# Kernel optimization log

Hardware: AMD Instinct MI355X
Metric: run time of the kernel (lower is better)

## Reference

```python
import jax, jax.numpy as jnp
import numpy as np

N, E, H, K = 50000, 300000, 128, 50
PI = float(np.pi)
EPS = 1e-5


def gaussian_expand(ea, k):
    # RBF expansion of each edge feature into k gaussians on [0, 1]
    centers = jnp.linspace(0.0, 1.0, k)            # (k,)
    width = 1.0 / k
    g = jnp.exp(-((ea[..., None] - centers) ** 2) / (2.0 * width * width))  # (E, 4, k)
    return g.reshape(ea.shape[0], -1)              # (E, 4k)


def bn_train(z, g, b):
    # BatchNorm1d in training mode: biased batch stats
    m = jnp.mean(z, axis=0)
    v = jnp.mean(z * z, axis=0) - m * m
    return (z - m) * jax.lax.rsqrt(v + EPS) * g + b


def lrelu(z):
    return jnp.where(z >= 0, z, 0.01 * z)


def setup_inputs() -> dict:
    key = jax.random.key(0)
    ks = jax.random.split(key, 16)
    s = 0.02
    d = {
        "x": jax.random.normal(ks[0], (N, H), jnp.float32),
        "edge_attr": jax.random.uniform(ks[1], (E, 4), jnp.float32),
        "edge_index": jax.random.randint(ks[2], (2, E), 0, N, jnp.int32),
        # f_b: Linear(4K -> H)
        "Wb": jax.random.normal(ks[3], (4 * K, H), jnp.float32) * s,
        "bb": jnp.zeros((H,), jnp.float32),
        # f_e: Linear(3H->H) + LReLU + BN + Linear(H->H) + LReLU + BN + Linear(H->H)
        "We1": jax.random.normal(ks[4], (3 * H, H), jnp.float32) * s,
        "be1": jnp.zeros((H,), jnp.float32),
        "ge1": jnp.ones((H,), jnp.float32),
        "bte1": jnp.zeros((H,), jnp.float32),
        "We2": jax.random.normal(ks[5], (H, H), jnp.float32) * s,
        "be2": jnp.zeros((H,), jnp.float32),
        "ge2": jnp.ones((H,), jnp.float32),
        "bte2": jnp.zeros((H,), jnp.float32),
        "We3": jax.random.normal(ks[6], (H, H), jnp.float32) * s,
        "be3": jnp.zeros((H,), jnp.float32),
        # f_d: Linear(H->H)
        "Wd": jax.random.normal(ks[7], (H, H), jnp.float32) * s,
        "bd": jnp.zeros((H,), jnp.float32),
        # v parameter (1, H)
        "v": jnp.ones((1, H), jnp.float32),
        # f_n: Linear(H->H) + LReLU + BN + Linear(H->H)
        "Wn1": jax.random.normal(ks[8], (H, H), jnp.float32) * s,
        "bn1": jnp.zeros((H,), jnp.float32),
        "gn": jnp.ones((H,), jnp.float32),
        "btn": jnp.zeros((H,), jnp.float32),
        "Wn2": jax.random.normal(ks[9], (H, H), jnp.float32) * s,
        "bn2": jnp.zeros((H,), jnp.float32),
    }
    return d


def reference(x, edge_attr, edge_index, Wb, bb, We1, be1, ge1, bte1, We2, be2,
              ge2, bte2, We3, be3, Wd, bd, v, Wn1, bn1, gn, btn, Wn2, bn2):
    src, dst = edge_index[0], edge_index[1]
    gt = gaussian_expand(edge_attr, K) @ Wb + bb            # (E, H)
    coeff = jnp.cos(PI / 2 * edge_attr[:, 3])[:, None]      # (E, 1)
    h = jnp.concatenate([x[src], gt, x[dst]], axis=1)       # (E, 3H)
    h = bn_train(lrelu(h @ We1 + be1), ge1, bte1)
    h = bn_train(lrelu(h @ We2 + be2), ge2, bte2)
    cond_filter = coeff * (h @ We3 + be3)                   # (E, H)
    m_st = cond_filter * (x[src] @ Wd + bd)                 # (E, H)
    m_t = v * (x @ Wd + bd)                                 # (N, H)
    incoming = jax.ops.segment_sum(m_st, dst, num_segments=N)  # scatter_add + zero pad
    z = m_t + incoming
    out = bn_train(lrelu(z @ Wn1 + bn1), gn, btn) @ Wn2 + bn2 + x
    return out
```

## Files before the change

kernel.cpp:

```cpp
#include <hip/hip_runtime.h>

typedef __attribute__((ext_vector_type(8))) short bf16x8;
typedef __attribute__((ext_vector_type(4))) float f32x4;

#define DEVFN __device__ __forceinline__

DEVFN short f2bf(float f) {
    union { float f; unsigned u; } v; v.f = f;
    unsigned r = (v.u + 0x7FFFu + ((v.u >> 16) & 1u)) >> 16;
    return (short)(unsigned short)r;
}
DEVFN float bf2f(short h) {
    union { unsigned u; float f; } v; v.u = ((unsigned)(unsigned short)h) << 16;
    return v.f;
}
DEVFN unsigned packbf(float a, float b) {
    return (unsigned)(unsigned short)f2bf(a) | ((unsigned)(unsigned short)f2bf(b) << 16);
}

#define GLD_LDS16(gp, lp)                                                     \
    __builtin_amdgcn_global_load_lds(                                         \
        (const __attribute__((address_space(1))) unsigned*)(gp),              \
        (__attribute__((address_space(3))) unsigned*)(lp), 16, 0, 0)



__global__ __launch_bounds__(128) void build_w1p_k(
    const float* __restrict__ Wb, const float* __restrict__ We1,
    const float* __restrict__ bb, const float* __restrict__ be1,
    float* __restrict__ W1p, float* __restrict__ b1p)
{
    int j = threadIdx.x;
    const float* B = We1 + 128 * 128;
    int i = blockIdx.x;
    if (i < 200) {
        float a = 0.f;
        for (int m = 0; m < 128; m++) a += Wb[i * 128 + m] * B[m * 128 + j];
        W1p[i * 128 + j] = a;
    } else {
        float a = be1[j];
        for (int m = 0; m < 128; m++) a += bb[m] * B[m * 128 + j];
        b1p[j] = a;
    }
}

__global__ __launch_bounds__(128) void build_tab_k(
    const float* __restrict__ W1p, const float* __restrict__ b1p,
    short* __restrict__ tab)
{
    int i = blockIdx.x;
    int c = blockIdx.y;
    int j = threadIdx.x;
    float t = (float)i * (1.0f / 1024.0f);
    float acc = (c == 0) ? b1p[j] : 0.f;
    int kc = (int)(t * 49.f + 0.5f);
    for (int dk = -6; dk <= 6; dk++) {
        int k = kc + dk;
        if (k >= 0 && k < 50) {
            float d = t - (float)k * (1.f / 49.f);
            float g = expf(-1250.f * d * d);
            acc += g * W1p[(c * 50 + k) * 128 + j];
        }
    }
    tab[((size_t)(c * 1025 + i)) * 128 + j] = f2bf(acc);
}

__global__ __launch_bounds__(256) void fold_plain_k(
    const float* __restrict__ W0, const float* __restrict__ W1,
    const float* __restrict__ W2, const float* __restrict__ W3,
    short* __restrict__ O0, short* __restrict__ O1,
    short* __restrict__ O2, short* __restrict__ O3)
{
    const float* W = (blockIdx.y == 0) ? W0 : (blockIdx.y == 1) ? W1 : (blockIdx.y == 2) ? W2 : W3;
    short* O = (blockIdx.y == 0) ? O0 : (blockIdx.y == 1) ? O1 : (blockIdx.y == 2) ? O2 : O3;
    int idx = blockIdx.x * 256 + threadIdx.x;
    int n = idx >> 8, ks = (idx >> 6) & 3, lane = idx & 63;
    int k8 = ks * 32 + (lane >> 4) * 8;
    int pcol = (lane & 15) * 8 + n;
    bf16x8 fv;
    #pragma unroll
    for (int i2 = 0; i2 < 8; i2++) fv[i2] = f2bf(W[(k8 + i2) * 128 + pcol]);
    *(bf16x8*)(O + (size_t)idx * 8) = fv;
}

__global__ __launch_bounds__(256) void fold_k(
    const float* __restrict__ W, const float* __restrict__ bias,
    const float* __restrict__ statsG, const float* __restrict__ gamma,
    const float* __restrict__ beta, float invNs,
    short* __restrict__ Bp, float* __restrict__ biasOut)
{
    __shared__ float sS[128], sT[128];
    int tid = threadIdx.x;
    if (tid < 128) {
        float sum = 0.f, sq = 0.f;
        for (int r = 0; r < 16; r++) {
            sum += statsG[r * 256 + tid];
            sq  += statsG[r * 256 + 128 + tid];
        }
        float m = sum * invNs;
        float var = sq * invNs - m * m;
        float rs = rsqrtf(var + 1e-5f);
        float s = rs * gamma[tid];
        float t = beta[tid] - m * s;
        sS[tid] = s; sT[tid] = t;
    }
    __syncthreads();
    if (blockIdx.x == 0 && tid < 128) {
        float b = bias[tid];
        for (int k = 0; k < 128; k++) b += sT[k] * W[k * 128 + tid];
        biasOut[tid] = b;
    }
    int idx = blockIdx.x * 256 + tid;
    int n = idx >> 8, ks = (idx >> 6) & 3, lane = idx & 63;
    int k8 = ks * 32 + (lane >> 4) * 8;
    int pcol = (lane & 15) * 8 + n;
    bf16x8 fv;
    #pragma unroll
    for (int i2 = 0; i2 < 8; i2++)
        fv[i2] = f2bf(sS[k8 + i2] * W[(k8 + i2) * 128 + pcol]);
    *(bf16x8*)(Bp + (size_t)idx * 8) = fv;
}


__global__ __launch_bounds__(256) void hist_k(
    const int* __restrict__ dstI, int* __restrict__ cnt, int E)
{
    int e = blockIdx.x * 256 + threadIdx.x;
    if (e < E) atomicAdd(&cnt[dstI[e]], 1);
}

__global__ __launch_bounds__(256) void scan1_k(
    const int* __restrict__ cnt, int Nn, int* __restrict__ posE, int* __restrict__ bsum)
{
    __shared__ int s[256];
    int t = threadIdx.x, g = blockIdx.x * 256 + t;
    int v = (g < Nn) ? cnt[g] : 0;
    s[t] = v;
    __syncthreads();
    for (int off = 1; off < 256; off <<= 1) {
        int u = (t >= off) ? s[t - off] : 0;
        __syncthreads();
        s[t] += u;
        __syncthreads();
    }
    if (g < Nn) posE[g] = s[t] - v;
    if (t == 255) bsum[blockIdx.x] = s[255];
}

__global__ __launch_bounds__(256) void scan2_k(int* __restrict__ bsum, int nb)
{
    __shared__ int s[256];
    int t = threadIdx.x;
    int v = (t < nb) ? bsum[t] : 0;
    s[t] = v;
    __syncthreads();
    for (int off = 1; off < 256; off <<= 1) {
        int u = (t >= off) ? s[t - off] : 0;
        __syncthreads();
        s[t] += u;
        __syncthreads();
    }
    if (t < nb) bsum[t] = s[t] - v;
}

__global__ __launch_bounds__(256) void fix_k(
    const int* __restrict__ posE, const int* __restrict__ bsum,
    int* __restrict__ pos2, int Nn)
{
    int id = blockIdx.x * 256 + threadIdx.x;
    if (id < Nn) pos2[id] = posE[id] + bsum[id >> 8];
}

__global__ __launch_bounds__(256) void scat_k(
    const int* __restrict__ srcI, const int* __restrict__ dstI,
    const float4* __restrict__ ea4, int* __restrict__ pos2,
    int* __restrict__ sSrc, int* __restrict__ sDst,
    float* __restrict__ scf, float4* __restrict__ sEa, int E)
{
    int e = blockIdx.x * 256 + threadIdx.x;
    if (e >= E) return;
    int d = dstI[e];
    int p = atomicAdd(&pos2[d], 1);
    sSrc[p] = srcI[e];
    sDst[p] = d;
    float4 ev = ea4[e];
    sEa[p] = ev;
    scf[p] = cosf(1.57079632679f * ev.w);
}

__global__ __launch_bounds__(256, 4) void node_all_k(
    const float* __restrict__ x, int M,
    const short* __restrict__ bp3,
    const float* __restrict__ bd, const float* __restrict__ vv,
    short* __restrict__ xd, short* __restrict__ zaccb,
    short* __restrict__ xs1b, short* __restrict__ xt1b)
{
    int tid = threadIdx.x;
    int wave = tid >> 6, lane = tid & 63;
    int kgrp = lane >> 4, colbase = lane & 15;
    int chunk = blockIdx.x;
    int rowA = chunk * 64 + wave * 16 + colbase;
    bool rv = rowA < M;

    bf16x8 af[4];
    #pragma unroll
    for (int ks = 0; ks < 4; ks++) {
        bf16x8 v = (bf16x8){0,0,0,0,0,0,0,0};
        if (rv) {
            const float* ap = x + (size_t)rowA * 128 + ks * 32 + kgrp * 8;
            float4 f0 = ((const float4*)ap)[0];
            float4 f1 = ((const float4*)ap)[1];
            v[0] = f2bf(f0.x); v[1] = f2bf(f0.y); v[2] = f2bf(f0.z); v[3] = f2bf(f0.w);
            v[4] = f2bf(f1.x); v[5] = f2bf(f1.y); v[6] = f2bf(f1.z); v[7] = f2bf(f1.w);
        }
        af[ks] = v;
    }

    float bcol[8], vcol[8];
    *(float4*)&bcol[0] = *(const float4*)(bd + colbase * 8);
    *(float4*)&bcol[4] = *(const float4*)(bd + colbase * 8 + 4);
    *(float4*)&vcol[0] = *(const float4*)(vv + colbase * 8);
    *(float4*)&vcol[4] = *(const float4*)(vv + colbase * 8 + 4);

    int rbase = chunk * 64 + wave * 16 + kgrp * 4;

    for (int b = 0; b < 3; b++) {
        const short* Bb = bp3 + (size_t)b * 16384;
        f32x4 acc[8];
        #pragma unroll
        for (int n = 0; n < 8; n++) acc[n] = (f32x4){0.f, 0.f, 0.f, 0.f};
        #pragma unroll
        for (int ks = 0; ks < 4; ks++) {
            #pragma unroll
            for (int n = 0; n < 8; n++) {
                bf16x8 bf = *(const bf16x8*)(Bb + ((size_t)((n * 4 + ks) * 64 + lane)) * 8);
                acc[n] = __builtin_amdgcn_mfma_f32_16x16x32_bf16(af[ks], bf, acc[n], 0, 0, 0);
            }
        }
        if (b == 0) {
            #pragma unroll
            for (int r = 0; r < 4; r++) {
                int row = rbase + r;
                if (row < M) {
                    bf16x8 xo, zo;
                    #pragma unroll
                    for (int n = 0; n < 8; n++) {
                        float val = acc[n][r] + bcol[n];
                        xo[n] = f2bf(val);
                        zo[n] = f2bf(vcol[n] * val);
                    }
                    *(bf16x8*)(xd    + (size_t)row * 128 + colbase * 8) = xo;
                    *(bf16x8*)(zaccb + (size_t)row * 128 + colbase * 8) = zo;
                }
            }
        } else {
            short* outp = (b == 1) ? xs1b : xt1b;
            #pragma unroll
            for (int r = 0; r < 4; r++) {
                int row = rbase + r;
                if (row < M) {
                    bf16x8 o;
                    #pragma unroll
                    for (int n = 0; n < 8; n++) o[n] = f2bf(acc[n][r]);
                    *(bf16x8*)(outp + (size_t)row * 128 + colbase * 8) = o;
                }
            }
        }
    }
}

__global__ __launch_bounds__(256) void edge_z1_k(
    const short* __restrict__ xs1b, const short* __restrict__ xt1b,
    const short* __restrict__ tab,
    const int* __restrict__ sSrc, const int* __restrict__ sDst,
    const float4* __restrict__ sEa,
    short* __restrict__ z1, float* __restrict__ stats, int Etot)
{
    int tid = threadIdx.x, wave = tid >> 6, lane = tid & 63;
    int colg = lane & 15, esub = lane >> 4;
    int e0 = blockIdx.x * 256 + wave * 64;

    int eL = e0 + lane;
    int myS = 0, myD = 0;
    float4 myE = {0.f, 0.f, 0.f, 0.f};
    if (eL < Etot) { myS = sSrc[eL]; myD = sDst[eL]; myE = sEa[eL]; }

    float sacc[8], qacc[8];
    #pragma unroll
    for (int j = 0; j < 8; j++) { sacc[j] = 0.f; qacc[j] = 0.f; }

    int ni = Etot - e0; if (ni > 64) ni = 64;
    int nsteps = (ni + 3) >> 2;

    for (int st = 0; st < nsteps; st++) {
        int i = st * 4 + esub;
        bool valid = i < ni;
        int s = __shfl(myS, i);
        int d = __shfl(myD, i);
        float tv[4];
        tv[0] = __shfl(myE.x, i); tv[1] = __shfl(myE.y, i);
        tv[2] = __shfl(myE.z, i); tv[3] = __shfl(myE.w, i);

        bf16x8 xs8 = *(const bf16x8*)(xs1b + (size_t)s * 128 + colg * 8);
        bf16x8 xt8 = *(const bf16x8*)(xt1b + (size_t)d * 128 + colg * 8);

        float p[8];
        #pragma unroll
        for (int j = 0; j < 8; j++) p[j] = bf2f(xs8[j]) + bf2f(xt8[j]);

        #pragma unroll
        for (int c = 0; c < 4; c++) {
            float u = tv[c] * 1024.f;
            int i0 = (int)u;
            if (i0 > 1023) i0 = 1023;
            if (i0 < 0) i0 = 0;
            float f = u - (float)i0;
            const short* tb = tab + ((size_t)(c * 1025 + i0)) * 128 + colg * 8;
            bf16x8 t0 = *(const bf16x8*)tb;
            bf16x8 t1 = *(const bf16x8*)(tb + 128);
            #pragma unroll
            for (int j = 0; j < 8; j++) {
                float v0 = bf2f(t0[j]);
                p[j] += v0 + f * (bf2f(t1[j]) - v0);
            }
        }

        bf16x8 o;
        #pragma unroll
        for (int j = 0; j < 8; j++) {
            float z = p[j] >= 0.f ? p[j] : 0.01f * p[j];
            o[j] = f2bf(z);
            if (valid) { sacc[j] += z; qacc[j] += z * z; }
        }
        if (valid)
            *(bf16x8*)(z1 + (size_t)(e0 + i) * 128 + colg * 8) = o;
    }

    __shared__ float lS[128], lQ[128];
    if (tid < 128) { lS[tid] = 0.f; lQ[tid] = 0.f; }
    __syncthreads();
    #pragma unroll
    for (int j = 0; j < 8; j++) {
        atomicAdd(&lS[colg * 8 + j], sacc[j]);
        atomicAdd(&lQ[colg * 8 + j], qacc[j]);
    }
    __syncthreads();
    if (tid < 128) {
        int rep = blockIdx.x & 15;
        atomicAdd(&stats[rep * 256 + tid], lS[tid]);
        atomicAdd(&stats[rep * 256 + 128 + tid], lQ[tid]);
    }
}

__global__ __launch_bounds__(256) void segred_k(
    const short* __restrict__ cond, const short* __restrict__ xd,
    const int* __restrict__ sSrc, const int* __restrict__ endPos,
    short* __restrict__ zaccb, int Nn)
{
    int tid = threadIdx.x, wave = tid >> 6, lane = tid & 63;
    int colg = lane & 7;
    int esub = lane >> 3;
    int d0 = blockIdx.x * 64 + wave * 16;

    for (int i = 0; i < 16; i++) {
        int d = d0 + i;
        if (d >= Nn) break;
        int s0 = (d == 0) ? 0 : endPos[d - 1];
        int s1 = endPos[d];
        if (s1 <= s0) continue;

        float acc[16];
        #pragma unroll
        for (int j = 0; j < 16; j++) acc[j] = 0.f;

        for (int t = s0 + esub; t < s1; t += 8) {
            const short* cp = cond + (size_t)t * 128 + colg * 16;
            bf16x8 c0 = *(const bf16x8*)cp;
            bf16x8 c1 = *(const bf16x8*)(cp + 8);
            int s = sSrc[t];
            const short* xp = xd + (size_t)s * 128 + colg * 16;
            bf16x8 x0 = *(const bf16x8*)xp;
            bf16x8 x1 = *(const bf16x8*)(xp + 8);
            #pragma unroll
            for (int j = 0; j < 8; j++) {
                acc[j]     += bf2f(c0[j]) * bf2f(x0[j]);
                acc[8 + j] += bf2f(c1[j]) * bf2f(x1[j]);
            }
        }

        #pragma unroll
        for (int j = 0; j < 16; j++) {
            acc[j] += __shfl_xor(acc[j], 8);
            acc[j] += __shfl_xor(acc[j], 16);
            acc[j] += __shfl_xor(acc[j], 32);
        }

        if (esub == 0) {
            short* zp = zaccb + (size_t)d * 128 + colg * 16;
            bf16x8 z0 = *(const bf16x8*)zp;
            bf16x8 z1 = *(const bf16x8*)(zp + 8);
            bf16x8 o0, o1;
            #pragma unroll
            for (int j = 0; j < 8; j++) {
                o0[j] = f2bf(bf2f(z0[j]) + acc[j]);
                o1[j] = f2bf(bf2f(z1[j]) + acc[8 + j]);
            }
            *(bf16x8*)zp = o0;
            *(bf16x8*)(zp + 8) = o1;
        }
    }
}

template<int EPI>
__global__ __launch_bounds__(256, 2) void pgemm_k(
    const short* __restrict__ A, int M,
    const short* __restrict__ Bp, const float* __restrict__ bias,
    void* __restrict__ out, float* __restrict__ stats,
    const short* __restrict__ xd, short* __restrict__ zaccb,
    const float* __restrict__ scf, const int* __restrict__ sSrc,
    const int* __restrict__ sDst, const float* __restrict__ xres)
{
    __shared__ __align__(16) short ldsB[16384];
    __shared__ float lS[128], lQ[128];
    int tid = threadIdx.x;
    int wave = tid >> 6, lane = tid & 63;
    int kgrp = lane >> 4, colbase = lane & 15;

    #pragma unroll
    for (int i = 0; i < 8; i++) {
        int off = (i * 256 + wave * 64 + lane) * 8;
        GLD_LDS16(Bp + off, ldsB + off);
    }

    int nch = (M + 63) >> 6;
    int c = blockIdx.x;

    bf16x8 afc[4];
    {
        int rowA = c * 64 + wave * 16 + colbase;
        bool rv = (c < nch) && (rowA < M);
        #pragma unroll
        for (int ks = 0; ks < 4; ks++)
            afc[ks] = rv ? *(const bf16x8*)(A + (size_t)rowA * 128 + ks * 32 + kgrp * 8)
                         : (bf16x8){0,0,0,0,0,0,0,0};
    }

    float bcol[8];
    *(float4*)&bcol[0] = *(const float4*)(bias + colbase * 8);
    *(float4*)&bcol[4] = *(const float4*)(bias + colbase * 8 + 4);

    float sreg[8], qreg[8];
    if (EPI == 2) {
        #pragma unroll
        for (int n = 0; n < 8; n++) { sreg[n] = 0.f; qreg[n] = 0.f; }
        if (tid < 128) { lS[tid] = 0.f; lQ[tid] = 0.f; }
    }

    __syncthreads();

    for (; c < nch; c += gridDim.x) {
        int cn = c + gridDim.x;
        bf16x8 afn[4];
        {
            int rowA = cn * 64 + wave * 16 + colbase;
            bool rv = (cn < nch) && (rowA < M);
            #pragma unroll
            for (int ks = 0; ks < 4; ks++)
                afn[ks] = rv ? *(const bf16x8*)(A + (size_t)rowA * 128 + ks * 32 + kgrp * 8)
                             : (bf16x8){0,0,0,0,0,0,0,0};
        }

        int rbase = c * 64 + wave * 16 + kgrp * 4;

        float mcf[4];
        if (EPI == 3) {
            #pragma unroll
            for (int r = 0; r < 4; r++) {
                int row = rbase + r;
                mcf[r] = (row < M) ? scf[row] : 0.f;
            }
        }

        f32x4 acc[8];
        #pragma unroll
        for (int n = 0; n < 8; n++) acc[n] = (f32x4){0.f, 0.f, 0.f, 0.f};
        #pragma unroll
        for (int ks = 0; ks < 4; ks++) {
            #pragma unroll
            for (int n = 0; n < 8; n++) {
                bf16x8 bf = *(const bf16x8*)(ldsB + ((size_t)((n * 4 + ks) * 64 + lane)) * 8);
                acc[n] = __builtin_amdgcn_mfma_f32_16x16x32_bf16(afc[ks], bf, acc[n], 0, 0, 0);
            }
        }

        if (EPI == 2) {
            short* outh = (short*)out;
            #pragma unroll
            for (int r = 0; r < 4; r++) {
                int row = rbase + r;
                bf16x8 o;
                #pragma unroll
                for (int n = 0; n < 8; n++) {
                    float z = acc[n][r] + bcol[n];
                    z = z >= 0.f ? z : 0.01f * z;
                    if (row >= M) z = 0.f;
                    sreg[n] += z; qreg[n] += z * z;
                    o[n] = f2bf(z);
                }
                if (row < M)
                    *(bf16x8*)(outh + (size_t)row * 128 + colbase * 8) = o;
            }
        } else if (EPI == 3) {
            short* outh = (short*)out;
            #pragma unroll
            for (int r = 0; r < 4; r++) {
                int row = rbase + r;
                if (row < M) {
                    bf16x8 o;
                    #pragma unroll
                    for (int n = 0; n < 8; n++)
                        o[n] = f2bf(mcf[r] * (acc[n][r] + bcol[n]));
                    *(bf16x8*)(outh + (size_t)row * 128 + colbase * 8) = o;
                }
            }
        } else if (EPI == 4) {
            float* outf = (float*)out;
            #pragma unroll
            for (int r = 0; r < 4; r++) {
                int row = rbase + r;
                if (row < M) {
                    const float4* xr = (const float4*)(xres + (size_t)row * 128 + colbase * 8);
                    float4 x0 = xr[0], x1 = xr[1];
                    float4 o0, o1;
                    o0.x = acc[0][r] + bcol[0] + x0.x;
                    o0.y = acc[1][r] + bcol[1] + x0.y;
                    o0.z = acc[2][r] + bcol[2] + x0.z;
                    o0.w = acc[3][r] + bcol[3] + x0.w;
                    o1.x = acc[4][r] + bcol[4] + x1.x;
                    o1.y = acc[5][r] + bcol[5] + x1.y;
                    o1.z = acc[6][r] + bcol[6] + x1.z;
                    o1.w = acc[7][r] + bcol[7] + x1.w;
                    float4* op = (float4*)(outf + (size_t)row * 128 + colbase * 8);
                    op[0] = o0; op[1] = o1;
                }
            }
        }

        #pragma unroll
        for (int ks = 0; ks < 4; ks++) afc[ks] = afn[ks];
    }

    if (EPI == 2) {
        __syncthreads();
        #pragma unroll
        for (int n = 0; n < 8; n++) {
            atomicAdd(&lS[colbase * 8 + n], sreg[n]);
            atomicAdd(&lQ[colbase * 8 + n], qreg[n]);
        }
        __syncthreads();
        if (tid < 128) {
            int rep = blockIdx.x & 15;
            atomicAdd(&stats[rep * 256 + tid], lS[tid]);
            atomicAdd(&stats[rep * 256 + 128 + tid], lQ[tid]);
        }
    }
}

extern "C" void kernel_launch(void* const* d_in, const int* in_sizes, int n_in,
                              void* d_out, int out_size, void* d_ws, size_t ws_size,
                              hipStream_t stream)
{
    const float* x    = (const float*)d_in[0];
    const float* ea   = (const float*)d_in[1];
    const int*   eidx = (const int*)d_in[2];
    const float* Wb   = (const float*)d_in[3];
    const float* bb   = (const float*)d_in[4];
    const float* We1  = (const float*)d_in[5];
    const float* be1  = (const float*)d_in[6];
    const float* ge1  = (const float*)d_in[7];
    const float* bte1 = (const float*)d_in[8];
    const float* We2  = (const float*)d_in[9];
    const float* be2  = (const float*)d_in[10];
    const float* ge2  = (const float*)d_in[11];
    const float* bte2 = (const float*)d_in[12];
    const float* We3  = (const float*)d_in[13];
    const float* be3  = (const float*)d_in[14];
    const float* Wd   = (const float*)d_in[15];
    const float* bd   = (const float*)d_in[16];
    const float* vv   = (const float*)d_in[17];
    const float* Wn1  = (const float*)d_in[18];
    const float* bn1  = (const float*)d_in[19];
    const float* gn   = (const float*)d_in[20];
    const float* btn  = (const float*)d_in[21];
    const float* Wn2  = (const float*)d_in[22];
    const float* bn2  = (const float*)d_in[23];

    const int NN = in_sizes[0] / 128;
    const int EE = in_sizes[1] / 4;

    char* ws = (char*)d_ws;
    size_t oEZ   = 0;
    size_t oXD   = oEZ   + (size_t)EE * 256;
    size_t oXS   = oXD   + (size_t)NN * 256;
    size_t oXT   = oXS   + (size_t)NN * 256;
    size_t oZACC = oXT   + (size_t)NN * 256;
    size_t oZN   = oZACC + (size_t)NN * 256;
    size_t oTAB  = oZN   + (size_t)NN * 256;
    size_t oW1P  = oTAB  + (size_t)4 * 1025 * 256;
    size_t oB1P  = oW1P  + (size_t)200 * 512;
    size_t oBP   = oB1P  + 512;
    size_t oBIAS = oBP   + (size_t)7 * 32768;
    size_t oST   = oBIAS + (size_t)7 * 512;
    size_t oCNT  = oST   + 49152;
    size_t oPOS  = oCNT  + 201728;
    size_t oBSUM = oPOS  + 201728;
    size_t oPOS2 = oBSUM + 1024;
    size_t oSSRC = oPOS2 + 201728;
    size_t oSDST = oSSRC + (size_t)EE * 4;
    size_t oSCF  = oSDST + (size_t)EE * 4;
    size_t oSEA  = (oSCF + (size_t)EE * 4 + 15) & ~(size_t)15;

    short* eZ    = (short*)(ws + oEZ);
    short* xd    = (short*)(ws + oXD);
    short* xs1b  = (short*)(ws + oXS);
    short* xt1b  = (short*)(ws + oXT);
    short* zaccb = (short*)(ws + oZACC);
    short* zn    = (short*)(ws + oZN);
    short* tab   = (short*)(ws + oTAB);
    float* W1p   = (float*)(ws + oW1P);
    float* b1p   = (float*)(ws + oB1P);
    short* bp    = (short*)(ws + oBP);
    short* BpW2  = bp + 3 * 16384;
    short* BpW3  = bp + 4 * 16384;
    short* BpN1  = bp + 5 * 16384;
    short* BpN2  = bp + 6 * 16384;
    float* bo    = (float*)(ws + oBIAS);
    float* b2p   = bo + 0 * 128;
    float* b3p   = bo + 1 * 128;
    float* b2np  = bo + 2 * 128;
    float* st1   = (float*)(ws + oST);
    float* st2   = st1 + 4096;
    float* stN   = st1 + 8192;
    int*   cnt   = (int*)(ws + oCNT);
    int*   posE  = (int*)(ws + oPOS);
    int*   bsum  = (int*)(ws + oBSUM);
    int*   pos2  = (int*)(ws + oPOS2);
    int*   sSrc  = (int*)(ws + oSSRC);
    int*   sDst  = (int*)(ws + oSDST);
    float* scf   = (float*)(ws + oSCF);
    float4* sEa  = (float4*)(ws + oSEA);

    hipMemsetAsync(ws + oST, 0, 49152 + 201728, stream);

    build_w1p_k<<<201, 128, 0, stream>>>(Wb, We1, bb, be1, W1p, b1p);
    build_tab_k<<<dim3(1025, 4), 128, 0, stream>>>(W1p, b1p, tab);
    fold_plain_k<<<dim3(8, 4), 256, 0, stream>>>(
        Wd, We1, We1 + 256 * 128, Wn1, bp, bp + 16384, bp + 2 * 16384, BpN1);

    int nchN = (NN + 63) / 64;
    int nchE = (EE + 63) / 64;
    int nbN = (NN + 255) / 256;
    int nbE = (EE + 255) / 256;
    int nbSeg = (NN + 63) / 64;

    int gridE = nchE < 1024 ? nchE : 1024;
    int gridN = nchN < 512 ? nchN : 512;

    node_all_k<<<nchN, 256, 0, stream>>>(x, NN, bp, bd, vv, xd, zaccb, xs1b, xt1b);

    hist_k<<<nbE, 256, 0, stream>>>(eidx + EE, cnt, EE);
    scan1_k<<<nbN, 256, 0, stream>>>(cnt, NN, posE, bsum);
    scan2_k<<<1, 256, 0, stream>>>(bsum, nbN);
    fix_k<<<nbN, 256, 0, stream>>>(posE, bsum, pos2, NN);
    scat_k<<<nbE, 256, 0, stream>>>(eidx, eidx + EE, (const float4*)ea, pos2,
                                    sSrc, sDst, scf, sEa, EE);

    edge_z1_k<<<nbE, 256, 0, stream>>>(xs1b, xt1b, tab, sSrc, sDst, sEa, eZ, st1, EE);

    fold_k<<<8, 256, 0, stream>>>(We2, be2, st1, ge1, bte1, 1.f / (float)EE, BpW2, b2p);
    pgemm_k<2><<<gridE, 256, 0, stream>>>(eZ, EE, BpW2, b2p, eZ, st2,
        nullptr, nullptr, nullptr, nullptr, nullptr, nullptr);

    fold_k<<<8, 256, 0, stream>>>(We3, be3, st2, ge2, bte2, 1.f / (float)EE, BpW3, b3p);
    pgemm_k<3><<<gridE, 256, 0, stream>>>(eZ, EE, BpW3, b3p, eZ, nullptr,
        nullptr, nullptr, scf, nullptr, nullptr, nullptr);

    segred_k<<<nbSeg, 256, 0, stream>>>(eZ, xd, sSrc, pos2, zaccb, NN);

    pgemm_k<2><<<gridN, 256, 0, stream>>>(zaccb, NN, BpN1, bn1, zn, stN,
        nullptr, nullptr, nullptr, nullptr, nullptr, nullptr);

    fold_k<<<8, 256, 0, stream>>>(Wn2, bn2, stN, gn, btn, 1.f / (float)NN, BpN2, b2np);
    pgemm_k<4><<<gridN, 256, 0, stream>>>(zn, NN, BpN2, b2np, d_out, nullptr,
        nullptr, nullptr, nullptr, nullptr, nullptr, x);
}
```

Measured before the change: 437.3 us.

## Pack interpolation table as value+delta, software-pipeline edge loads, use packed bf16 convert

The Gaussian lookup table now stores each entry as a bf16 value paired with a bf16 delta to the next entry. Each interpolation therefore needs one contiguous 32-bit fetch per column instead of two separate row reads, and the lerp becomes a single fma. The edge_z1 kernel double-buffers its gathers, issuing loads for the next edge step before consuming the current one to hide gather latency. It also reads indices directly instead of through shuffles. Output packing in this kernel and the GEMM epilogues switches to the hardware v_cvt_pk_bf16_f32 instruction, at the cost of more registers and slightly different rounding of the delta.

```diff
diff --git a/kernel.cpp b/kernel.cpp
--- a/kernel.cpp
+++ b/kernel.cpp
@@ -2,6 +2,7 @@
 
 typedef __attribute__((ext_vector_type(8))) short bf16x8;
 typedef __attribute__((ext_vector_type(4))) float f32x4;
+typedef __attribute__((ext_vector_type(4))) unsigned uint32x4;
 
 #define DEVFN __device__ __forceinline__
 
@@ -14,8 +15,10 @@
     union { unsigned u; float f; } v; v.u = ((unsigned)(unsigned short)h) << 16;
     return v.f;
 }
-DEVFN unsigned packbf(float a, float b) {
-    return (unsigned)(unsigned short)f2bf(a) | ((unsigned)(unsigned short)f2bf(b) << 16);
+DEVFN unsigned pkbf(float a, float b) {
+    unsigned r;
+    asm("v_cvt_pk_bf16_f32 %0, %1, %2" : "=v"(r) : "v"(a), "v"(b));
+    return r;
 }
 
 #define GLD_LDS16(gp, lp)                                                     \
@@ -46,23 +49,31 @@
 
 __global__ __launch_bounds__(128) void build_tab_k(
     const float* __restrict__ W1p, const float* __restrict__ b1p,
-    short* __restrict__ tab)
+    unsigned* __restrict__ tabP)
 {
     int i = blockIdx.x;
     int c = blockIdx.y;
     int j = threadIdx.x;
-    float t = (float)i * (1.0f / 1024.0f);
-    float acc = (c == 0) ? b1p[j] : 0.f;
-    int kc = (int)(t * 49.f + 0.5f);
-    for (int dk = -6; dk <= 6; dk++) {
+    float t0 = (float)i * (1.0f / 1024.0f);
+    float t1 = (float)(i + 1) * (1.0f / 1024.0f);
+    float base = (c == 0) ? b1p[j] : 0.f;
+    float a0 = base, a1 = base;
+    int kc = (int)(t0 * 49.f + 0.5f);
+    for (int dk = -6; dk <= 7; dk++) {
         int k = kc + dk;
         if (k >= 0 && k < 50) {
-            float d = t - (float)k * (1.f / 49.f);
-            float g = expf(-1250.f * d * d);
-            acc += g * W1p[(c * 50 + k) * 128 + j];
-        }
-    }
-    tab[((size_t)(c * 1025 + i)) * 128 + j] = f2bf(acc);
+            float w = W1p[(c * 50 + k) * 128 + j];
+            float d0 = t0 - (float)k * (1.f / 49.f);
+            float d1 = t1 - (float)k * (1.f / 49.f);
+            a0 += expf(-1250.f * d0 * d0) * w;
+            a1 += expf(-1250.f * d1 * d1) * w;
+        }
+    }
+    float v0 = bf2f(f2bf(a0));
+    float v1 = bf2f(f2bf(a1));
+    unsigned lo = (unsigned)(unsigned short)f2bf(a0);
+    unsigned hi = (unsigned)(unsigned short)f2bf(v1 - v0);
+    tabP[((size_t)(c * 1024 + i)) * 128 + j] = lo | (hi << 16);
 }
 
 __global__ __launch_bounds__(256) void fold_plain_k(
@@ -269,9 +280,65 @@
     }
 }
 
+
+#define EZ_ISSUE(XS, XT, TA, TB, FV, slot) do {                                \
+    int e_ = e0 + (slot);                                                      \
+    int ec_ = e_ < Etot ? e_ : Etot - 1;                                       \
+    int s_ = sSrc[ec_];                                                        \
+    int d_ = sDst[ec_];                                                        \
+    float4 ea_ = sEa[ec_];                                                     \
+    XS = *(const bf16x8*)(xs1b + (size_t)s_ * 128 + colg * 8);                 \
+    XT = *(const bf16x8*)(xt1b + (size_t)d_ * 128 + colg * 8);                 \
+    float tv_[4] = {ea_.x, ea_.y, ea_.z, ea_.w};                               \
+    _Pragma("unroll")                                                          \
+    for (int c_ = 0; c_ < 4; c_++) {                                           \
+        float u_ = tv_[c_] * 1024.f;                                           \
+        int i0_ = (int)u_;                                                     \
+        i0_ = i0_ < 0 ? 0 : (i0_ > 1023 ? 1023 : i0_);                         \
+        FV[c_] = u_ - (float)i0_;                                              \
+        const uint32x4* tp_ = (const uint32x4*)(tabP +                         \
+            ((size_t)(c_ * 1024 + i0_) * 128) + colg * 8);                     \
+        TA[c_] = tp_[0];                                                       \
+        TB[c_] = tp_[1];                                                       \
+    }                                                                          \
+} while (0)
+
+#define EZ_CONSUME(XS, XT, TA, TB, FV, slot) do {                              \
+    float p_[8];                                                               \
+    _Pragma("unroll")                                                          \
+    for (int j_ = 0; j_ < 8; j_++) p_[j_] = bf2f(XS[j_]) + bf2f(XT[j_]);       \
+    _Pragma("unroll")                                                          \
+    for (int c_ = 0; c_ < 4; c_++) {                                           \
+        float f_ = FV[c_];                                                     \
+        _Pragma("unroll")                                                      \
+        for (int j_ = 0; j_ < 4; j_++) {                                       \
+            unsigned ua_ = TA[c_][j_];                                         \
+            p_[j_] = fmaf(f_, __uint_as_float(ua_ & 0xffff0000u),              \
+                          p_[j_] + __uint_as_float(ua_ << 16));                \
+            unsigned ub_ = TB[c_][j_];                                         \
+            p_[j_ + 4] = fmaf(f_, __uint_as_float(ub_ & 0xffff0000u),          \
+                              p_[j_ + 4] + __uint_as_float(ub_ << 16));        \
+        }                                                                      \
+    }                                                                          \
+    bool valid_ = (slot) < ni;                                                 \
+    _Pragma("unroll")                                                          \
+    for (int j_ = 0; j_ < 8; j_++) {                                           \
+        float z_ = p_[j_] >= 0.f ? p_[j_] : 0.01f * p_[j_];                    \
+        p_[j_] = z_;                                                           \
+        float m_ = valid_ ? z_ : 0.f;                                          \
+        sacc[j_] += m_;                                                        \
+        qacc[j_] = fmaf(m_, z_, qacc[j_]);                                     \
+    }                                                                          \
+    if (valid_) {                                                              \
+        uint32x4 ov_ = {pkbf(p_[0], p_[1]), pkbf(p_[2], p_[3]),                \
+                        pkbf(p_[4], p_[5]), pkbf(p_[6], p_[7])};               \
+        *(uint32x4*)(z1 + (size_t)(e0 + (slot)) * 128 + colg * 8) = ov_;       \
+    }                                                                          \
+} while (0)
+
 __global__ __launch_bounds__(256) void edge_z1_k(
     const short* __restrict__ xs1b, const short* __restrict__ xt1b,
-    const short* __restrict__ tab,
+    const unsigned* __restrict__ tabP,
     const int* __restrict__ sSrc, const int* __restrict__ sDst,
     const float4* __restrict__ sEa,
     short* __restrict__ z1, float* __restrict__ stats, int Etot)
@@ -280,61 +347,28 @@
     int colg = lane & 15, esub = lane >> 4;
     int e0 = blockIdx.x * 256 + wave * 64;
 
-    int eL = e0 + lane;
-    int myS = 0, myD = 0;
-    float4 myE = {0.f, 0.f, 0.f, 0.f};
-    if (eL < Etot) { myS = sSrc[eL]; myD = sDst[eL]; myE = sEa[eL]; }
-
     float sacc[8], qacc[8];
     #pragma unroll
     for (int j = 0; j < 8; j++) { sacc[j] = 0.f; qacc[j] = 0.f; }
 
-    int ni = Etot - e0; if (ni > 64) ni = 64;
+    int ni = Etot - e0;
+    if (ni > 64) ni = 64;
+    if (ni < 0) ni = 0;
     int nsteps = (ni + 3) >> 2;
 
-    for (int st = 0; st < nsteps; st++) {
-        int i = st * 4 + esub;
-        bool valid = i < ni;
-        int s = __shfl(myS, i);
-        int d = __shfl(myD, i);
-        float tv[4];
-        tv[0] = __shfl(myE.x, i); tv[1] = __shfl(myE.y, i);
-        tv[2] = __shfl(myE.z, i); tv[3] = __shfl(myE.w, i);
-
-        bf16x8 xs8 = *(const bf16x8*)(xs1b + (size_t)s * 128 + colg * 8);
-        bf16x8 xt8 = *(const bf16x8*)(xt1b + (size_t)d * 128 + colg * 8);
-
-        float p[8];
-        #pragma unroll
-        for (int j = 0; j < 8; j++) p[j] = bf2f(xs8[j]) + bf2f(xt8[j]);
-
-        #pragma unroll
-        for (int c = 0; c < 4; c++) {
-            float u = tv[c] * 1024.f;
-            int i0 = (int)u;
-            if (i0 > 1023) i0 = 1023;
-            if (i0 < 0) i0 = 0;
-            float f = u - (float)i0;
-            const short* tb = tab + ((size_t)(c * 1025 + i0)) * 128 + colg * 8;
-            bf16x8 t0 = *(const bf16x8*)tb;
-            bf16x8 t1 = *(const bf16x8*)(tb + 128);
-            #pragma unroll
-            for (int j = 0; j < 8; j++) {
-                float v0 = bf2f(t0[j]);
-                p[j] += v0 + f * (bf2f(t1[j]) - v0);
-            }
-        }
-
-        bf16x8 o;
-        #pragma unroll
-        for (int j = 0; j < 8; j++) {
-            float z = p[j] >= 0.f ? p[j] : 0.01f * p[j];
-            o[j] = f2bf(z);
-            if (valid) { sacc[j] += z; qacc[j] += z * z; }
-        }
-        if (valid)
-            *(bf16x8*)(z1 + (size_t)(e0 + i) * 128 + colg * 8) = o;
-    }
+    bf16x8 xsA, xtA; uint32x4 taA[4], tbA[4]; float fvA[4];
+    bf16x8 xsB, xtB; uint32x4 taB[4], tbB[4]; float fvB[4];
+
+    EZ_ISSUE(xsA, xtA, taA, tbA, fvA, esub);
+    int st = 0;
+    for (; st + 2 <= nsteps; st += 2) {
+        EZ_ISSUE(xsB, xtB, taB, tbB, fvB, (st + 1) * 4 + esub);
+        EZ_CONSUME(xsA, xtA, taA, tbA, fvA, st * 4 + esub);
+        EZ_ISSUE(xsA, xtA, taA, tbA, fvA, (st + 2) * 4 + esub);
+        EZ_CONSUME(xsB, xtB, taB, tbB, fvB, (st + 1) * 4 + esub);
+    }
+    if (st < nsteps)
+        EZ_CONSUME(xsA, xtA, taA, tbA, fvA, st * 4 + esub);
 
     __shared__ float lS[128], lQ[128];
     if (tid < 128) { lS[tid] = 0.f; lQ[tid] = 0.f; }
@@ -498,17 +532,20 @@
             #pragma unroll
             for (int r = 0; r < 4; r++) {
                 int row = rbase + r;
-                bf16x8 o;
+                float zz[8];
                 #pragma unroll
                 for (int n = 0; n < 8; n++) {
                     float z = acc[n][r] + bcol[n];
                     z = z >= 0.f ? z : 0.01f * z;
                     if (row >= M) z = 0.f;
                     sreg[n] += z; qreg[n] += z * z;
-                    o[n] = f2bf(z);
+                    zz[n] = z;
                 }
-                if (row < M)
-                    *(bf16x8*)(outh + (size_t)row * 128 + colbase * 8) = o;
+                if (row < M) {
+                    uint32x4 ov = {pkbf(zz[0], zz[1]), pkbf(zz[2], zz[3]),
+                                   pkbf(zz[4], zz[5]), pkbf(zz[6], zz[7])};
+                    *(uint32x4*)(outh + (size_t)row * 128 + colbase * 8) = ov;
+                }
             }
         } else if (EPI == 3) {
             short* outh = (short*)out;
@@ -516,11 +553,13 @@
             for (int r = 0; r < 4; r++) {
                 int row = rbase + r;
                 if (row < M) {
-                    bf16x8 o;
+                    float zz[8];
                     #pragma unroll
                     for (int n = 0; n < 8; n++)
-                        o[n] = f2bf(mcf[r] * (acc[n][r] + bcol[n]));
-                    *(bf16x8*)(outh + (size_t)row * 128 + colbase * 8) = o;
+                        zz[n] = mcf[r] * (acc[n][r] + bcol[n]);
+                    uint32x4 ov = {pkbf(zz[0], zz[1]), pkbf(zz[2], zz[3]),
+                                   pkbf(zz[4], zz[5]), pkbf(zz[6], zz[7])};
+                    *(uint32x4*)(outh + (size_t)row * 128 + colbase * 8) = ov;
                 }
             }
         } else if (EPI == 4) {
@@ -606,7 +645,7 @@
     size_t oZACC = oXT   + (size_t)NN * 256;
     size_t oZN   = oZACC + (size_t)NN * 256;
     size_t oTAB  = oZN   + (size_t)NN * 256;
-    size_t oW1P  = oTAB  + (size_t)4 * 1025 * 256;
+    size_t oW1P  = oTAB  + (size_t)4 * 1024 * 512;
     size_t oB1P  = oW1P  + (size_t)200 * 512;
     size_t oBP   = oB1P  + 512;
     size_t oBIAS = oBP   + (size_t)7 * 32768;
@@ -626,7 +665,7 @@
     short* xt1b  = (short*)(ws + oXT);
     short* zaccb = (short*)(ws + oZACC);
     short* zn    = (short*)(ws + oZN);
-    short* tab   = (short*)(ws + oTAB);
+    unsigned* tabP = (unsigned*)(ws + oTAB);
     float* W1p   = (float*)(ws + oW1P);
     float* b1p   = (float*)(ws + oB1P);
     short* bp    = (short*)(ws + oBP);
@@ -653,7 +692,7 @@
     hipMemsetAsync(ws + oST, 0, 49152 + 201728, stream);
 
     build_w1p_k<<<201, 128, 0, stream>>>(Wb, We1, bb, be1, W1p, b1p);
-    build_tab_k<<<dim3(1025, 4), 128, 0, stream>>>(W1p, b1p, tab);
+    build_tab_k<<<dim3(1024, 4), 128, 0, stream>>>(W1p, b1p, tabP);
     fold_plain_k<<<dim3(8, 4), 256, 0, stream>>>(
         Wd, We1, We1 + 256 * 128, Wn1, bp, bp + 16384, bp + 2 * 16384, BpN1);
 
@@ -675,7 +714,7 @@
     scat_k<<<nbE, 256, 0, stream>>>(eidx, eidx + EE, (const float4*)ea, pos2,
                                     sSrc, sDst, scf, sEa, EE);
 
-    edge_z1_k<<<nbE, 256, 0, stream>>>(xs1b, xt1b, tab, sSrc, sDst, sEa, eZ, st1, EE);
+    edge_z1_k<<<nbE, 256, 0, stream>>>(xs1b, xt1b, tabP, sSrc, sDst, sEa, eZ, st1, EE);
 
     fold_k<<<8, 256, 0, stream>>>(We2, be2, st1, ge1, bte1, 1.f / (float)EE, BpW2, b2p);
     pgemm_k<2><<<gridE, 256, 0, stream>>>(eZ, EE, BpW2, b2p, eZ, st2,
```

New measurement: 423.9 us. 1.03x faster.
